# Kernel optimization log

Measured on AMD Instinct MI355X. Metric: run time of the kernel, lower is better.

## Reference

```python
import jax, jax.numpy as jnp
import numpy as np

N, C_IN, C_RED, H, W = 16, 256, 64, 48, 48


def conv1x1(x, w, b):
    # x: [N, Cin, H, W], w: [Cout, Cin], b: [Cout]
    return jnp.einsum('nchw,oc->nohw', x, w) + b[None, :, None, None]


def setup_inputs() -> dict:
    key = jax.random.key(0)
    ks = jax.random.split(key, 10)
    s_in = 1.0 / np.sqrt(C_IN)
    s_red = 1.0 / np.sqrt(C_RED)
    return {
        'feature_maps': jax.random.normal(ks[0], (N, C_IN, H, W), jnp.float32),
        'global_channel_output': jax.random.normal(ks[1], (N, C_IN, H, W), jnp.float32),
        'Wq': jax.random.uniform(ks[2], (C_RED, C_IN), jnp.float32, -s_in, s_in),
        'bq': jax.random.uniform(ks[3], (C_RED,), jnp.float32, -s_in, s_in),
        'Wk': jax.random.uniform(ks[4], (C_RED, C_IN), jnp.float32, -s_in, s_in),
        'bk': jax.random.uniform(ks[5], (C_RED,), jnp.float32, -s_in, s_in),
        'Wv': jax.random.uniform(ks[6], (C_RED, C_IN), jnp.float32, -s_in, s_in),
        'bv': jax.random.uniform(ks[7], (C_RED,), jnp.float32, -s_in, s_in),
        'Watt': jax.random.uniform(ks[8], (C_IN, C_RED), jnp.float32, -s_red, s_red),
        'batt': jax.random.uniform(ks[9], (C_IN,), jnp.float32, -s_red, s_red),
    }


def reference(feature_maps, global_channel_output, Wq, bq, Wk, bk, Wv, bv, Watt, batt):
    n, _, h, w = feature_maps.shape
    hw = h * w
    q = conv1x1(feature_maps, Wq, bq).reshape(n, -1, hw)   # [N, Cr, HW]
    k = conv1x1(feature_maps, Wk, bk).reshape(n, -1, hw)   # [N, Cr, HW]
    v = conv1x1(feature_maps, Wv, bv).reshape(n, -1, hw)   # [N, Cr, HW]
    # key^T @ query -> [N, HW, HW]
    qk = jnp.einsum('nci,ncj->nij', k, q)
    # global (flattened) softmax over the whole HWxHW matrix per batch element
    qk = jax.nn.softmax(qk.reshape(n, hw * hw), axis=-1).reshape(n, hw, hw)
    att = jnp.einsum('nci,nij->ncj', v, qk).reshape(n, -1, h, w)  # [N, Cr, H, W]
    att = conv1x1(att, Watt, batt)                                 # [N, Cin, H, W]
    return global_channel_output * att + global_channel_output
```

## Files before the change

### kernel.cpp

```cpp
#include <hip/hip_runtime.h>
#include <hip/hip_bf16.h>
#include <stdint.h>

#define NB   16
#define CIN  256
#define CRED 64
#define HW   2304
#define JT_ATT  128
#define NJT_ATT 18
#define NIG  4
#define NIT  9

typedef __bf16 bf16;
typedef __bf16 bf16x8 __attribute__((ext_vector_type(8)));
typedef __bf16 bf16x4 __attribute__((ext_vector_type(4)));
typedef float  f32x4  __attribute__((ext_vector_type(4)));

__global__ __launch_bounds__(256) void prep_kernel(
    const float* __restrict__ Wq, const float* __restrict__ bq,
    const float* __restrict__ Wk, const float* __restrict__ Wv,
    const float* __restrict__ Watt,
    bf16* __restrict__ Wqb, bf16* __restrict__ Wkb, bf16* __restrict__ Wvb,
    bf16* __restrict__ Wab, float* __restrict__ bqs)
{
    const float INVLN2 = 1.44269504088896f;
    int i = blockIdx.x * 256 + threadIdx.x;
    Wqb[i] = (bf16)(Wq[i] * INVLN2);
    Wkb[i] = (bf16)Wk[i];
    Wvb[i] = (bf16)Wv[i];
    Wab[i] = (bf16)Watt[i];
    if (i < CRED) bqs[i] = bq[i] * INVLN2;
}

__global__ __launch_bounds__(256) void qkv_kernel(
    const float* __restrict__ x,
    const bf16* __restrict__ Wqb, const float* __restrict__ bqs,
    const bf16* __restrict__ Wkb, const float* __restrict__ bk,
    const bf16* __restrict__ Wvb, const float* __restrict__ bv,
    bf16* __restrict__ qT, bf16* __restrict__ kT, bf16* __restrict__ v)
{
    __shared__ __align__(16) bf16 sX[32 * 264];
    const int jt = blockIdx.x, n = blockIdx.y;
    const int jbase = jt * 32;
    const int tid = threadIdx.x;
    const int lane = tid & 63, w = tid >> 6;
    const int l15 = lane & 15, q4 = lane >> 4;

    const float* xn = x + ((size_t)n * CIN) * HW + jbase;
    #pragma unroll
    for (int it = 0; it < 8; ++it) {
        int idx = tid + 256 * it;
        int c = idx >> 3, p4 = idx & 7;
        const float4 vv = *(const float4*)(xn + c * HW + p4 * 4);
        sX[(p4 * 4 + 0) * 264 + c] = (bf16)vv.x;
        sX[(p4 * 4 + 1) * 264 + c] = (bf16)vv.y;
        sX[(p4 * 4 + 2) * 264 + c] = (bf16)vv.z;
        sX[(p4 * 4 + 3) * 264 + c] = (bf16)vv.w;
    }
    __syncthreads();

    const bf16*  Ws[3] = {Wqb, Wkb, Wvb};
    const float* bs[3] = {bqs, bk, bv};
    #pragma unroll
    for (int wi = 0; wi < 3; ++wi) {
        bf16x8 a[8];
        const bf16* Wp = Ws[wi] + (w * 16 + l15) * CIN + q4 * 8;
        #pragma unroll
        for (int ks = 0; ks < 8; ++ks) a[ks] = *(const bf16x8*)(Wp + ks * 32);
        f32x4 acc[2] = {};
        #pragma unroll
        for (int nt = 0; nt < 2; ++nt) {
            #pragma unroll
            for (int ks = 0; ks < 8; ++ks) {
                bf16x8 b = *(const bf16x8*)(sX + (nt * 16 + l15) * 264 + ks * 32 + q4 * 8);
                acc[nt] = __builtin_amdgcn_mfma_f32_16x16x32_bf16(a[ks], b, acc[nt], 0, 0, 0);
            }
        }
        const int crb = w * 16 + q4 * 4;
        const float b0 = bs[wi][crb], b1 = bs[wi][crb + 1],
                    b2 = bs[wi][crb + 2], b3 = bs[wi][crb + 3];
        if (wi < 2) {
            bf16* dst = (wi == 0 ? qT : kT) + ((size_t)n * HW) * 64;
            #pragma unroll
            for (int nt = 0; nt < 2; ++nt) {
                int pos = jbase + nt * 16 + l15;
                bf16x4 pk = {(bf16)(acc[nt].x + b0), (bf16)(acc[nt].y + b1),
                             (bf16)(acc[nt].z + b2), (bf16)(acc[nt].w + b3)};
                *(bf16x4*)(dst + pos * 64 + crb) = pk;
            }
        } else {
            bf16* dst = v + ((size_t)n * CRED) * HW;
            #pragma unroll
            for (int nt = 0; nt < 2; ++nt) {
                int pos = jbase + nt * 16 + l15;
                dst[(crb + 0) * HW + pos] = (bf16)(acc[nt].x + b0);
                dst[(crb + 1) * HW + pos] = (bf16)(acc[nt].y + b1);
                dst[(crb + 2) * HW + pos] = (bf16)(acc[nt].z + b2);
                dst[(crb + 3) * HW + pos] = (bf16)(acc[nt].w + b3);
            }
        }
    }
}

__global__ __launch_bounds__(256, 4) void attn_kernel(
    const bf16* __restrict__ qT, const bf16* __restrict__ kT,
    const bf16* __restrict__ v,
    float* __restrict__ OTp, float* __restrict__ Z)
{
    __shared__ __align__(16) bf16 sK[2][64 * 72];
    __shared__ __align__(16) bf16 sV[2][64 * 72];
    const int jt = blockIdx.x, ig = blockIdx.y, n = blockIdx.z;
    const int jbase = jt * JT_ATT;
    const int tid = threadIdx.x;
    const int lane = tid & 63, w = tid >> 6;
    const int l15 = lane & 15, q4 = lane >> 4;

    bf16x8 qf[2][2];
    {
        const bf16* qn = qT + ((size_t)n * HW + jbase + w * 32) * 64;
        #pragma unroll
        for (int nt = 0; nt < 2; ++nt)
            #pragma unroll
            for (int ks = 0; ks < 2; ++ks)
                qf[nt][ks] = *(const bf16x8*)(qn + (nt * 16 + l15) * 64 + ks * 32 + q4 * 8);
    }

    f32x4 oacc[4][2] = {};
    float zacc = 0.f;
    const uint4* ksrc = (const uint4*)(kT + ((size_t)n * HW) * 64);
    const bf16* vbase = v + ((size_t)n * CRED) * HW;

    const int r0 = tid >> 3, c0 = tid & 7;
    const int ibase0 = ig * NIT * 64;
    const int pbase = ((c0 >> 2) & 1) * 32 + (c0 & 1) * 16 + ((c0 >> 1) & 1) * 4;

    uint4 kr0 = ksrc[(ibase0 + r0) * 8 + c0];
    uint4 kr1 = ksrc[(ibase0 + r0 + 32) * 8 + c0];
    uint4 vr0 = *(const uint4*)(vbase + (size_t)r0 * HW + ibase0 + c0 * 8);
    uint4 vr1 = *(const uint4*)(vbase + (size_t)(r0 + 32) * HW + ibase0 + c0 * 8);

    auto stage = [&](int buf) {
        uint4* dk = (uint4*)sK[buf];
        dk[r0 * 9 + c0] = kr0;
        dk[(r0 + 32) * 9 + c0] = kr1;
        bf16* dv0 = sV[buf] + r0 * 72 + pbase;
        bf16* dv1 = sV[buf] + (r0 + 32) * 72 + pbase;
        uint2 t;
        t.x = vr0.x; t.y = vr0.y; *(uint2*)(dv0)     = t;
        t.x = vr0.z; t.y = vr0.w; *(uint2*)(dv0 + 8) = t;
        t.x = vr1.x; t.y = vr1.y; *(uint2*)(dv1)     = t;
        t.x = vr1.z; t.y = vr1.w; *(uint2*)(dv1 + 8) = t;
    };

    stage(0);
    {
        const int nb = ibase0 + ((1 < NIT) ? 64 : 0);
        kr0 = ksrc[(nb + r0) * 8 + c0];
        kr1 = ksrc[(nb + r0 + 32) * 8 + c0];
        vr0 = *(const uint4*)(vbase + (size_t)r0 * HW + nb + c0 * 8);
        vr1 = *(const uint4*)(vbase + (size_t)(r0 + 32) * HW + nb + c0 * 8);
    }
    __syncthreads();

    for (int it = 0; it < NIT; ++it) {
        const int cur = it & 1;
        const bf16* K = sK[cur];
        const bf16* V = sV[cur];

        unsigned pw[2][4][2];
        #pragma unroll
        for (int is = 0; is < 4; ++is) {
            bf16x8 kf0 = *(const bf16x8*)(K + (is * 16 + l15) * 72 + q4 * 8);
            bf16x8 kf1 = *(const bf16x8*)(K + (is * 16 + l15) * 72 + 32 + q4 * 8);
            #pragma unroll
            for (int nt = 0; nt < 2; ++nt) {
                f32x4 s = {};
                s = __builtin_amdgcn_mfma_f32_16x16x32_bf16(kf0, qf[nt][0], s, 0, 0, 0);
                s = __builtin_amdgcn_mfma_f32_16x16x32_bf16(kf1, qf[nt][1], s, 0, 0, 0);
                float p0 = exp2f(s.x), p1 = exp2f(s.y);
                float p2 = exp2f(s.z), p3 = exp2f(s.w);
                zacc += (p0 + p1) + (p2 + p3);
                unsigned w0, w1;
                asm("v_cvt_pk_bf16_f32 %0, %1, %2" : "=v"(w0) : "v"(p0), "v"(p1));
                asm("v_cvt_pk_bf16_f32 %0, %1, %2" : "=v"(w1) : "v"(p2), "v"(p3));
                pw[nt][is][0] = w0;
                pw[nt][is][1] = w1;
            }
        }
        #pragma unroll
        for (int g = 0; g < 2; ++g) {
            bf16x8 vf[4];
            #pragma unroll
            for (int ct = 0; ct < 4; ++ct)
                vf[ct] = *(const bf16x8*)(V + (ct * 16 + l15) * 72 + g * 32 + q4 * 8);
            #pragma unroll
            for (int nt = 0; nt < 2; ++nt) {
                union { unsigned u[4]; bf16x8 v8; } pb;
                pb.u[0] = pw[nt][2 * g][0];
                pb.u[1] = pw[nt][2 * g][1];
                pb.u[2] = pw[nt][2 * g + 1][0];
                pb.u[3] = pw[nt][2 * g + 1][1];
                #pragma unroll
                for (int ct = 0; ct < 4; ++ct)
                    oacc[ct][nt] = __builtin_amdgcn_mfma_f32_16x16x32_bf16(
                        vf[ct], pb.v8, oacc[ct][nt], 0, 0, 0);
            }
        }

        if (it + 1 < NIT) {
            stage(cur ^ 1);
            const int nb = ibase0 + ((it + 2 < NIT) ? (it + 2) * 64 : 0);
            kr0 = ksrc[(nb + r0) * 8 + c0];
            kr1 = ksrc[(nb + r0 + 32) * 8 + c0];
            vr0 = *(const uint4*)(vbase + (size_t)r0 * HW + nb + c0 * 8);
            vr1 = *(const uint4*)(vbase + (size_t)(r0 + 32) * HW + nb + c0 * 8);
            __syncthreads();
        }
    }
    float* OTn = OTp + (((size_t)ig * NB + n) * HW) * 64;
    #pragma unroll
    for (int ct = 0; ct < 4; ++ct)
        #pragma unroll
        for (int nt = 0; nt < 2; ++nt) {
            int pos = jbase + w * 32 + nt * 16 + l15;
            *(f32x4*)(OTn + (size_t)pos * 64 + ct * 16 + q4 * 4) = oacc[ct][nt];
        }
    #pragma unroll
    for (int off = 32; off > 0; off >>= 1) zacc += __shfl_down(zacc, off);
    if (lane == 0) atomicAdd(Z + n, zacc);
}

__global__ __launch_bounds__(256) void out_kernel(
    const float* __restrict__ OTp, const float* __restrict__ Z,
    const bf16* __restrict__ Wab, const float* __restrict__ batt,
    const float* __restrict__ g, float* __restrict__ out)
{
    __shared__ __align__(16) bf16 sO[32 * 72];
    const int jt = blockIdx.x, n = blockIdx.y;
    const int jbase = jt * 32;
    const int tid = threadIdx.x;
    const int lane = tid & 63, w = tid >> 6;
    const int l15 = lane & 15, q4 = lane >> 4;
    const float invZ = 1.0f / Z[n];

    #pragma unroll
    for (int i0 = 0; i0 < 2; ++i0) {
        int i = tid + i0 * 256;
        int r = i >> 4, c4 = i & 15;
        const float* p = OTp + (((size_t)n * HW) + jbase + r) * 64 + c4 * 4;
        float4 s = *(const float4*)(p);
        #pragma unroll
        for (int igx = 1; igx < NIG; ++igx) {
            float4 t = *(const float4*)(p + (size_t)igx * NB * HW * 64);
            s.x += t.x; s.y += t.y; s.z += t.z; s.w += t.w;
        }
        bf16x4 pk = {(bf16)(s.x * invZ), (bf16)(s.y * invZ),
                     (bf16)(s.z * invZ), (bf16)(s.w * invZ)};
        *(bf16x4*)(sO + r * 72 + c4 * 4) = pk;
    }
    __syncthreads();

    bf16x8 bfr[2][2];
    #pragma unroll
    for (int nt = 0; nt < 2; ++nt)
        #pragma unroll
        for (int ks = 0; ks < 2; ++ks)
            bfr[nt][ks] = *(const bf16x8*)(sO + (nt * 16 + l15) * 72 + ks * 32 + q4 * 8);

    const float* gp = g + ((size_t)n * CIN) * HW;
    float* op = out + ((size_t)n * CIN) * HW;
    #pragma unroll
    for (int mt = 0; mt < 4; ++mt) {
        const bf16* Wp = Wab + (w * 64 + mt * 16 + l15) * 64 + q4 * 8;
        bf16x8 a0 = *(const bf16x8*)(Wp);
        bf16x8 a1 = *(const bf16x8*)(Wp + 32);
        const int co = w * 64 + mt * 16 + q4 * 4;
        const float c0 = batt[co], c1 = batt[co + 1], c2 = batt[co + 2], c3 = batt[co + 3];
        #pragma unroll
        for (int nt = 0; nt < 2; ++nt) {
            f32x4 acc = {};
            acc = __builtin_amdgcn_mfma_f32_16x16x32_bf16(a0, bfr[nt][0], acc, 0, 0, 0);
            acc = __builtin_amdgcn_mfma_f32_16x16x32_bf16(a1, bfr[nt][1], acc, 0, 0, 0);
            const int pos = jbase + nt * 16 + l15;
            const float g0 = gp[(co + 0) * HW + pos], g1 = gp[(co + 1) * HW + pos];
            const float g2 = gp[(co + 2) * HW + pos], g3 = gp[(co + 3) * HW + pos];
            op[(co + 0) * HW + pos] = g0 * (acc.x + c0 + 1.0f);
            op[(co + 1) * HW + pos] = g1 * (acc.y + c1 + 1.0f);
            op[(co + 2) * HW + pos] = g2 * (acc.z + c2 + 1.0f);
            op[(co + 3) * HW + pos] = g3 * (acc.w + c3 + 1.0f);
        }
    }
}

extern "C" void kernel_launch(void* const* d_in, const int* in_sizes, int n_in,
                              void* d_out, int out_size, void* d_ws, size_t ws_size,
                              hipStream_t stream) {
    const float* x    = (const float*)d_in[0];
    const float* g    = (const float*)d_in[1];
    const float* Wq   = (const float*)d_in[2];
    const float* bq   = (const float*)d_in[3];
    const float* Wk   = (const float*)d_in[4];
    const float* bk   = (const float*)d_in[5];
    const float* Wv   = (const float*)d_in[6];
    const float* bv   = (const float*)d_in[7];
    const float* Watt = (const float*)d_in[8];
    const float* batt = (const float*)d_in[9];
    float* out = (float*)d_out;

    char* ws = (char*)d_ws;
    const size_t qkv_sz = (size_t)NB * HW * CRED * sizeof(bf16);
    bf16*  qT  = (bf16*)(ws);
    bf16*  kT  = (bf16*)(ws + qkv_sz);
    bf16*  vv  = (bf16*)(ws + 2 * qkv_sz);
    float* OTp = (float*)(ws + 3 * qkv_sz);
    char*  w2  = ws + 3 * qkv_sz + (size_t)NIG * NB * HW * CRED * sizeof(float);
    float* Zp  = (float*)(w2);
    bf16*  Wqb = (bf16*)(w2 + 256);
    bf16*  Wkb = Wqb + CRED * CIN;
    bf16*  Wvb = Wkb + CRED * CIN;
    bf16*  Wab = Wvb + CRED * CIN;
    float* bqs = (float*)(Wab + CIN * CRED);

    hipMemsetAsync(Zp, 0, NB * sizeof(float), stream);

    dim3 blk(256);
    prep_kernel<<<dim3(64), blk, 0, stream>>>(Wq, bq, Wk, Wv, Watt, Wqb, Wkb, Wvb, Wab, bqs);
    qkv_kernel<<<dim3(HW / 32, NB), blk, 0, stream>>>(x, Wqb, bqs, Wkb, bk, Wvb, bv, qT, kT, vv);
    attn_kernel<<<dim3(NJT_ATT, NIG, NB), blk, 0, stream>>>(qT, kT, vv, OTp, Zp);
    out_kernel<<<dim3(HW / 32, NB), blk, 0, stream>>>(OTp, Zp, Wab, batt, g, out);
}
```

Before: 246.7 us.

## Load K/V fragments directly from global memory and remap blocks across XCDs

Measured after the change: 324.7 us. +31.6%, slower.

```diff
diff --git a/kernel.cpp b/kernel.cpp
--- a/kernel.cpp
+++ b/kernel.cpp
@@ -102,22 +102,24 @@
     }
 }
 
-__global__ __launch_bounds__(256, 4) void attn_kernel(
+__global__ __launch_bounds__(256, 3) void attn_kernel(
     const bf16* __restrict__ qT, const bf16* __restrict__ kT,
     const bf16* __restrict__ v,
     float* __restrict__ OTp, float* __restrict__ Z)
 {
-    __shared__ __align__(16) bf16 sK[2][64 * 72];
-    __shared__ __align__(16) bf16 sV[2][64 * 72];
-    const int jt = blockIdx.x, ig = blockIdx.y, n = blockIdx.z;
-    const int jbase = jt * JT_ATT;
+    const int phys = blockIdx.x;
+    const int virt = (phys & 7) * 144 + (phys >> 3);
+    const int jt = virt % NJT_ATT;
+    const int ig = (virt / NJT_ATT) & 3;
+    const int n  = virt / (NJT_ATT * NIG);
     const int tid = threadIdx.x;
     const int lane = tid & 63, w = tid >> 6;
     const int l15 = lane & 15, q4 = lane >> 4;
+    const int jb = jt * JT_ATT + w * 32;
 
     bf16x8 qf[2][2];
     {
-        const bf16* qn = qT + ((size_t)n * HW + jbase + w * 32) * 64;
+        const bf16* qn = qT + ((size_t)n * HW + jb) * 64;
         #pragma unroll
         for (int nt = 0; nt < 2; ++nt)
             #pragma unroll
@@ -127,94 +129,95 @@
 
     f32x4 oacc[4][2] = {};
     float zacc = 0.f;
-    const uint4* ksrc = (const uint4*)(kT + ((size_t)n * HW) * 64);
-    const bf16* vbase = v + ((size_t)n * CRED) * HW;
-
-    const int r0 = tid >> 3, c0 = tid & 7;
+    const bf16* kb = kT + ((size_t)n * HW) * 64;
+    const bf16* vb = v + ((size_t)n * CRED) * HW;
     const int ibase0 = ig * NIT * 64;
-    const int pbase = ((c0 >> 2) & 1) * 32 + (c0 & 1) * 16 + ((c0 >> 1) & 1) * 4;
-
-    uint4 kr0 = ksrc[(ibase0 + r0) * 8 + c0];
-    uint4 kr1 = ksrc[(ibase0 + r0 + 32) * 8 + c0];
-    uint4 vr0 = *(const uint4*)(vbase + (size_t)r0 * HW + ibase0 + c0 * 8);
-    uint4 vr1 = *(const uint4*)(vbase + (size_t)(r0 + 32) * HW + ibase0 + c0 * 8);
-
-    auto stage = [&](int buf) {
-        uint4* dk = (uint4*)sK[buf];
-        dk[r0 * 9 + c0] = kr0;
-        dk[(r0 + 32) * 9 + c0] = kr1;
-        bf16* dv0 = sV[buf] + r0 * 72 + pbase;
-        bf16* dv1 = sV[buf] + (r0 + 32) * 72 + pbase;
-        uint2 t;
-        t.x = vr0.x; t.y = vr0.y; *(uint2*)(dv0)     = t;
-        t.x = vr0.z; t.y = vr0.w; *(uint2*)(dv0 + 8) = t;
-        t.x = vr1.x; t.y = vr1.y; *(uint2*)(dv1)     = t;
-        t.x = vr1.z; t.y = vr1.w; *(uint2*)(dv1 + 8) = t;
-    };
-
-    stage(0);
-    {
-        const int nb = ibase0 + ((1 < NIT) ? 64 : 0);
-        kr0 = ksrc[(nb + r0) * 8 + c0];
-        kr1 = ksrc[(nb + r0 + 32) * 8 + c0];
-        vr0 = *(const uint4*)(vbase + (size_t)r0 * HW + nb + c0 * 8);
-        vr1 = *(const uint4*)(vbase + (size_t)(r0 + 32) * HW + nb + c0 * 8);
-    }
-    __syncthreads();
 
     for (int it = 0; it < NIT; ++it) {
-        const int cur = it & 1;
-        const bf16* K = sK[cur];
-        const bf16* V = sV[cur];
+        const int ibase = ibase0 + it * 64;
+
+        bf16x8 kf[4][2];
+        #pragma unroll
+        for (int is = 0; is < 4; ++is) {
+            const bf16* kp = kb + (size_t)(ibase + is * 16 + l15) * 64 + q4 * 8;
+            kf[is][0] = *(const bf16x8*)(kp);
+            kf[is][1] = *(const bf16x8*)(kp + 32);
+        }
+        bf16x8 vf0[4];
+        #pragma unroll
+        for (int ct = 0; ct < 4; ++ct) {
+            const bf16* vp = vb + (size_t)(ct * 16 + l15) * HW + ibase + q4 * 4;
+            union { uint32_t u[4]; bf16x8 v8; } t;
+            uint2 a0 = *(const uint2*)(vp);
+            uint2 a1 = *(const uint2*)(vp + 16);
+            t.u[0] = a0.x; t.u[1] = a0.y; t.u[2] = a1.x; t.u[3] = a1.y;
+            vf0[ct] = t.v8;
+        }
 
         unsigned pw[2][4][2];
         #pragma unroll
-        for (int is = 0; is < 4; ++is) {
-            bf16x8 kf0 = *(const bf16x8*)(K + (is * 16 + l15) * 72 + q4 * 8);
-            bf16x8 kf1 = *(const bf16x8*)(K + (is * 16 + l15) * 72 + 32 + q4 * 8);
+        for (int is = 0; is < 2; ++is) {
             #pragma unroll
             for (int nt = 0; nt < 2; ++nt) {
                 f32x4 s = {};
-                s = __builtin_amdgcn_mfma_f32_16x16x32_bf16(kf0, qf[nt][0], s, 0, 0, 0);
-                s = __builtin_amdgcn_mfma_f32_16x16x32_bf16(kf1, qf[nt][1], s, 0, 0, 0);
-                float p0 = exp2f(s.x), p1 = exp2f(s.y);
-                float p2 = exp2f(s.z), p3 = exp2f(s.w);
+                s = __builtin_amdgcn_mfma_f32_16x16x32_bf16(kf[is][0], qf[nt][0], s, 0, 0, 0);
+                s = __builtin_amdgcn_mfma_f32_16x16x32_bf16(kf[is][1], qf[nt][1], s, 0, 0, 0);
+                float p0, p1, p2, p3;
+                asm("v_exp_f32 %0, %1" : "=v"(p0) : "v"(s.x));
+                asm("v_exp_f32 %0, %1" : "=v"(p1) : "v"(s.y));
+                asm("v_exp_f32 %0, %1" : "=v"(p2) : "v"(s.z));
+                asm("v_exp_f32 %0, %1" : "=v"(p3) : "v"(s.w));
                 zacc += (p0 + p1) + (p2 + p3);
-                unsigned w0, w1;
-                asm("v_cvt_pk_bf16_f32 %0, %1, %2" : "=v"(w0) : "v"(p0), "v"(p1));
-                asm("v_cvt_pk_bf16_f32 %0, %1, %2" : "=v"(w1) : "v"(p2), "v"(p3));
-                pw[nt][is][0] = w0;
-                pw[nt][is][1] = w1;
-            }
-        }
-        #pragma unroll
-        for (int g = 0; g < 2; ++g) {
-            bf16x8 vf[4];
+                asm("v_cvt_pk_bf16_f32 %0, %1, %2" : "=v"(pw[nt][is][0]) : "v"(p0), "v"(p1));
+                asm("v_cvt_pk_bf16_f32 %0, %1, %2" : "=v"(pw[nt][is][1]) : "v"(p2), "v"(p3));
+            }
+        }
+        bf16x8 vf1[4];
+        #pragma unroll
+        for (int ct = 0; ct < 4; ++ct) {
+            const bf16* vp = vb + (size_t)(ct * 16 + l15) * HW + ibase + 32 + q4 * 4;
+            union { uint32_t u[4]; bf16x8 v8; } t;
+            uint2 a0 = *(const uint2*)(vp);
+            uint2 a1 = *(const uint2*)(vp + 16);
+            t.u[0] = a0.x; t.u[1] = a0.y; t.u[2] = a1.x; t.u[3] = a1.y;
+            vf1[ct] = t.v8;
+        }
+        #pragma unroll
+        for (int nt = 0; nt < 2; ++nt) {
+            union { unsigned u[4]; bf16x8 v8; } pb;
+            pb.u[0] = pw[nt][0][0]; pb.u[1] = pw[nt][0][1];
+            pb.u[2] = pw[nt][1][0]; pb.u[3] = pw[nt][1][1];
             #pragma unroll
             for (int ct = 0; ct < 4; ++ct)
-                vf[ct] = *(const bf16x8*)(V + (ct * 16 + l15) * 72 + g * 32 + q4 * 8);
+                oacc[ct][nt] = __builtin_amdgcn_mfma_f32_16x16x32_bf16(
+                    vf0[ct], pb.v8, oacc[ct][nt], 0, 0, 0);
+        }
+        #pragma unroll
+        for (int is = 2; is < 4; ++is) {
             #pragma unroll
             for (int nt = 0; nt < 2; ++nt) {
-                union { unsigned u[4]; bf16x8 v8; } pb;
-                pb.u[0] = pw[nt][2 * g][0];
-                pb.u[1] = pw[nt][2 * g][1];
-                pb.u[2] = pw[nt][2 * g + 1][0];
-                pb.u[3] = pw[nt][2 * g + 1][1];
-                #pragma unroll
-                for (int ct = 0; ct < 4; ++ct)
-                    oacc[ct][nt] = __builtin_amdgcn_mfma_f32_16x16x32_bf16(
-                        vf[ct], pb.v8, oacc[ct][nt], 0, 0, 0);
-            }
-        }
-
-        if (it + 1 < NIT) {
-            stage(cur ^ 1);
-            const int nb = ibase0 + ((it + 2 < NIT) ? (it + 2) * 64 : 0);
-            kr0 = ksrc[(nb + r0) * 8 + c0];
-            kr1 = ksrc[(nb + r0 + 32) * 8 + c0];
-            vr0 = *(const uint4*)(vbase + (size_t)r0 * HW + nb + c0 * 8);
-            vr1 = *(const uint4*)(vbase + (size_t)(r0 + 32) * HW + nb + c0 * 8);
-            __syncthreads();
+                f32x4 s = {};
+                s = __builtin_amdgcn_mfma_f32_16x16x32_bf16(kf[is][0], qf[nt][0], s, 0, 0, 0);
+                s = __builtin_amdgcn_mfma_f32_16x16x32_bf16(kf[is][1], qf[nt][1], s, 0, 0, 0);
+                float p0, p1, p2, p3;
+                asm("v_exp_f32 %0, %1" : "=v"(p0) : "v"(s.x));
+                asm("v_exp_f32 %0, %1" : "=v"(p1) : "v"(s.y));
+                asm("v_exp_f32 %0, %1" : "=v"(p2) : "v"(s.z));
+                asm("v_exp_f32 %0, %1" : "=v"(p3) : "v"(s.w));
+                zacc += (p0 + p1) + (p2 + p3);
+                asm("v_cvt_pk_bf16_f32 %0, %1, %2" : "=v"(pw[nt][is][0]) : "v"(p0), "v"(p1));
+                asm("v_cvt_pk_bf16_f32 %0, %1, %2" : "=v"(pw[nt][is][1]) : "v"(p2), "v"(p3));
+            }
+        }
+        #pragma unroll
+        for (int nt = 0; nt < 2; ++nt) {
+            union { unsigned u[4]; bf16x8 v8; } pb;
+            pb.u[0] = pw[nt][2][0]; pb.u[1] = pw[nt][2][1];
+            pb.u[2] = pw[nt][3][0]; pb.u[3] = pw[nt][3][1];
+            #pragma unroll
+            for (int ct = 0; ct < 4; ++ct)
+                oacc[ct][nt] = __builtin_amdgcn_mfma_f32_16x16x32_bf16(
+                    vf1[ct], pb.v8, oacc[ct][nt], 0, 0, 0);
         }
     }
     float* OTn = OTp + (((size_t)ig * NB + n) * HW) * 64;
@@ -222,7 +225,7 @@
     for (int ct = 0; ct < 4; ++ct)
         #pragma unroll
         for (int nt = 0; nt < 2; ++nt) {
-            int pos = jbase + w * 32 + nt * 16 + l15;
+            int pos = jb + nt * 16 + l15;
             *(f32x4*)(OTn + (size_t)pos * 64 + ct * 16 + q4 * 4) = oacc[ct][nt];
         }
     #pragma unroll
@@ -326,6 +329,6 @@
     dim3 blk(256);
     prep_kernel<<<dim3(64), blk, 0, stream>>>(Wq, bq, Wk, Wv, Watt, Wqb, Wkb, Wvb, Wab, bqs);
     qkv_kernel<<<dim3(HW / 32, NB), blk, 0, stream>>>(x, Wqb, bqs, Wkb, bk, Wvb, bv, qT, kT, vv);
-    attn_kernel<<<dim3(NJT_ATT, NIG, NB), blk, 0, stream>>>(qT, kT, vv, OTp, Zp);
+    attn_kernel<<<dim3(NJT_ATT * NIG * NB), blk, 0, stream>>>(qT, kT, vv, OTp, Zp);
     out_kernel<<<dim3(HW / 32, NB), blk, 0, stream>>>(OTp, Zp, Wab, batt, g, out);
 }
```
